# Kernel tuning notes

Hardware: AMD Instinct MI355X
Metric: run time of the kernel (lower is better)

## Reference

```python
import jax, jax.numpy as jnp
import numpy as np

C_IN, C_OUT = 256, 128

def setup_inputs() -> dict:
    key = jax.random.key(0)
    k1, k2, k3, k4, k5, k6 = jax.random.split(key, 6)
    B, H, W = 8, 64, 64
    p = jax.random.normal(k1, (B, C_IN, H, W), dtype=jnp.float32)
    b = jax.random.normal(k2, (B, C_IN, H, W), dtype=jnp.float32)
    # 1x1 conv weights (Conv2d with kernel 1 == pointwise matmul) + biases
    sq = 1.0 / np.sqrt(C_IN)
    Wq = jax.random.uniform(k3, (C_OUT, C_IN), jnp.float32, -sq, sq)
    bq = jax.random.uniform(k4, (C_OUT,), jnp.float32, -sq, sq)
    Wk = jax.random.uniform(k5, (C_OUT, C_IN), jnp.float32, -sq, sq)
    bk = jax.random.uniform(k6, (C_OUT,), jnp.float32, -sq, sq)
    return {"p": p, "b": b, "Wq": Wq, "bq": bq, "Wk": Wk, "bk": bk}

def reference(p, b, Wq, bq, Wk, bk):
    B, C, H, W = p.shape
    N = H * W
    # 1x1 convs -> flatten spatial dim to N
    q = jnp.einsum('bchw,oc->bhwo', p, Wq) + bq          # [B,H,W,Co]
    q = q.reshape(B, N, -1).astype(jnp.float32)           # [B,N,Co] (query permuted)
    k = jnp.einsum('bchw,oc->bohw', b, Wk) + bk[None, :, None, None]
    k = k.reshape(B, -1, N).astype(jnp.float32)           # [B,Co,N]
    energy = jnp.einsum('bnc,bcm->bnm', q, k)             # [B,N,N] unscaled
    attention = jax.nn.softmax(energy, axis=-1)           # softmax over keys
    value = b.reshape(B, C, N)                            # [B,C,N]
    out = jnp.einsum('bnm,bcm->bcn', attention, value)    # [B,C,N]
    return out.reshape(B, C, H, W)
```

## Files before the change

kernel.cpp:

```cpp
#include <hip/hip_runtime.h>
#include <hip/hip_bf16.h>
#include <math.h>


#define B_   8
#define CIN  256
#define COUT 128
#define NN   4096

typedef _Float16 half8  __attribute__((ext_vector_type(8)));
typedef short    short8 __attribute__((ext_vector_type(8)));
typedef float    f32x4  __attribute__((ext_vector_type(4)));

#define LOG2E 1.44269504088896340736f

__device__ __forceinline__ unsigned short f2bf(float f) {
    union { float f; unsigned u; } v; v.f = f;
    return (unsigned short)((v.u + 0x7FFFu + ((v.u >> 16) & 1u)) >> 16);
}
__device__ __forceinline__ unsigned short f2h(float f) {
    union { _Float16 h; unsigned short u; } v; v.h = (_Float16)f;
    return v.u;
}
__device__ __forceinline__ unsigned int packbf2(float lo, float hi) {
    return (unsigned int)f2bf(lo) | ((unsigned int)f2bf(hi) << 16);
}
__device__ __forceinline__ void dma16(void* lds, const void* g) {
    __builtin_amdgcn_global_load_lds(
        (const __attribute__((address_space(1))) unsigned int*)g,
        (__attribute__((address_space(3))) unsigned int*)lds,
        16, 0, 0);
}

__global__ __launch_bounds__(256) void cvt_w(const float* __restrict__ Wq,
                                             const float* __restrict__ Wk,
                                             const float* __restrict__ bq,
                                             _Float16* __restrict__ Whq,
                                             _Float16* __restrict__ Whk,
                                             float* __restrict__ bqs) {
    const int bx = blockIdx.x, t = threadIdx.x;
    const int isK = (bx >= 32);
    const float* src = isK ? Wk : Wq;
    _Float16* dst = isK ? Whk : Whq;
    const float scale = isK ? 1.0f : LOG2E;
    const int idx = (bx & 31) * 256 + t;
    float4 v = ((const float4*)src)[idx];
    unsigned long long pk = (unsigned long long)f2h(v.x * scale)
                          | ((unsigned long long)f2h(v.y * scale) << 16)
                          | ((unsigned long long)f2h(v.z * scale) << 32)
                          | ((unsigned long long)f2h(v.w * scale) << 48);
    ((unsigned long long*)dst)[idx] = pk;
    if (bx == 0 && t < COUT) bqs[t] = bq[t] * LOG2E;
}

__global__ __launch_bounds__(256) void proj3(const float* __restrict__ X,
                                             const _Float16* __restrict__ Wh,
                                             const float* __restrict__ bias,
                                             _Float16* __restrict__ outN,
                                             _Float16* __restrict__ outT,
                                             unsigned short* __restrict__ Vb)
{
    __shared__ __align__(16) unsigned short T[64 * 264];
    const int bx = blockIdx.x, b = bx >> 6, n0 = (bx & 63) << 6;
    const int t  = threadIdx.x;
    const int cr = t >> 2;
    const int nch = (t & 3) << 4;

#pragma unroll
    for (int it = 0; it < 4; ++it) {
        const int c = it * 64 + cr;
        const float* src = X + ((size_t)(b * CIN + c) * NN + n0 + nch);
        float v[16];
#pragma unroll
        for (int k = 0; k < 4; ++k) {
            float4 f = *(const float4*)(src + k * 4);
            v[k*4] = f.x; v[k*4+1] = f.y; v[k*4+2] = f.z; v[k*4+3] = f.w;
        }
#pragma unroll
        for (int j = 0; j < 16; ++j) T[(nch + j) * 264 + c] = f2h(v[j]);
        if (Vb) {
            unsigned short o[16];
#pragma unroll
            for (int j = 0; j < 16; ++j) o[j] = f2bf(v[j]);
            unsigned short* dst = Vb + (size_t)(b * CIN + c) * NN + n0 + nch;
            *(int4*)dst = *(int4*)o;
            *(int4*)(dst + 8) = *(int4*)(o + 8);
        }
    }
    __syncthreads();

    const int w = t >> 6, lane = t & 63, l15 = lane & 15, quad = lane >> 4, q8 = quad * 8;
    half8 a[8];
#pragma unroll
    for (int s = 0; s < 8; ++s)
        a[s] = *(const half8*)&T[(w * 16 + l15) * 264 + s * 32 + q8];
    f32x4 D[8];
#pragma unroll
    for (int og = 0; og < 8; ++og) D[og] = (f32x4){0.f, 0.f, 0.f, 0.f};
#pragma unroll
    for (int s = 0; s < 8; ++s) {
        const _Float16* wp = Wh + (size_t)l15 * CIN + s * 32 + q8;
#pragma unroll
        for (int og = 0; og < 8; ++og) {
            half8 wf = *(const half8*)(wp + og * 16 * CIN);
            D[og] = __builtin_amdgcn_mfma_f32_16x16x32_f16(a[s], wf, D[og], 0, 0, 0);
        }
    }
    const int nrow = n0 + w * 16 + quad * 4;
    if (outT) {
#pragma unroll
        for (int og = 0; og < 8; ++og) {
            const int o = og * 16 + l15;
            const float bo = bias[o];
            const int c = o >> 3, j = o & 7;
            const int sw = (c & 7) << 2;
#pragma unroll
            for (int r2 = 0; r2 < 4; ++r2) {
                const int n = nrow + r2;
                const int tile = n >> 5, m = n & 31;
                const size_t pos = ((size_t)(b * 128 + tile) * 512
                                    + c * 32 + ((m + sw) & 31)) * 8 + j;
                outT[pos] = (_Float16)(D[og][r2] + bo);
            }
        }
    } else {
#pragma unroll
        for (int og = 0; og < 8; ++og) {
            const int o = og * 16 + l15;
            const float bo = bias[o];
            _Float16* op = outN + ((size_t)(b * NN + nrow) * COUT + o);
#pragma unroll
            for (int r2 = 0; r2 < 4; ++r2)
                op[(size_t)r2 * COUT] = (_Float16)(D[og][r2] + bo);
        }
    }
}

__global__ __launch_bounds__(256, 2) void flash_kernel(const _Float16* __restrict__ Q,
                                                       const _Float16* __restrict__ Ktt,
                                                       const unsigned short* __restrict__ V,
                                                       float* __restrict__ out) {
    __shared__ __align__(16) _Float16       K0sh[32 * 128];
    __shared__ __align__(16) _Float16       K1sh[32 * 128];
    __shared__ __align__(16) unsigned short V0sh[256 * 32];
    __shared__ __align__(16) unsigned short V1sh[256 * 32];
    __shared__ __align__(16) unsigned short Psh[64 * 40];
    __shared__ __align__(16) float          Lsh[64];

    const int bx   = blockIdx.x;
    const int b    = bx >> 6;
    const int q0   = (bx & 63) << 6;
    const int t    = threadIdx.x;
    const int w    = t >> 6;
    const int lane = t & 63;
    const int l15  = lane & 15;
    const int quad = lane >> 4;
    const int q8   = quad * 8;

    const _Float16* Qg = Q + (size_t)b * NN * COUT;
    const _Float16* Kb = Ktt + (size_t)b * 128 * 4096;
    const unsigned short* Vg = V + (size_t)b * CIN * NN;

    half8 Qf[4];
    {
        const _Float16* qr = Qg + (size_t)(q0 + w * 16 + l15) * COUT;
#pragma unroll
        for (int s = 0; s < 4; ++s)
            Qf[s] = *(const half8*)(qr + s * 32 + q8);
    }

    f32x4 O[16];
#pragma unroll
    for (int i = 0; i < 16; ++i) O[i] = (f32x4){0.f, 0.f, 0.f, 0.f};
    float lsum[4] = {0.f, 0.f, 0.f, 0.f};

    const int vmq   = ((lane & 3) - ((lane >> 3) & 3)) & 3;
    const int vcrow = lane >> 2;
    const int vslot = (quad + (l15 >> 1)) & 3;

    auto issueK = [&](int kt, _Float16* Kd) {
        const _Float16* gk = Kb + (size_t)kt * 4096;
        dma16(Kd + (w * 2 + 0) * 512, gk + (w * 2 + 0) * 512 + lane * 8);
        dma16(Kd + (w * 2 + 1) * 512, gk + (w * 2 + 1) * 512 + lane * 8);
    };
    auto issueV = [&](int kt, unsigned short* Vd) {
        const int k0 = kt << 5;
#pragma unroll
        for (int i = 0; i < 4; ++i) {
            const int cc = (w * 4 + i) * 16 + vcrow;
            dma16(Vd + (w * 4 + i) * 512,
                  Vg + (size_t)cc * NN + k0 + vmq * 8);
        }
    };

    auto halfstep = [&](int kt, const _Float16* Kc, const unsigned short* Vc,
                        _Float16* Kn, unsigned short* Vn) {
        if (kt + 1 < 128) issueK(kt + 1, Kn);

        f32x4 S0 = {0.f, 0.f, 0.f, 0.f}, S1 = {0.f, 0.f, 0.f, 0.f};
#pragma unroll
        for (int s = 0; s < 4; ++s) {
            const int kc = 4 * s + quad;
            const int sw = (kc & 7) << 2;
            const int x0 = (l15 + sw) & 31;
            half8 kf0 = *(const half8*)(Kc + (kc * 32 + x0) * 8);
            half8 kf1 = *(const half8*)(Kc + (kc * 32 + (x0 ^ 16)) * 8);
            S0 = __builtin_amdgcn_mfma_f32_16x16x32_f16(Qf[s], kf0, S0, 0, 0, 0);
            S1 = __builtin_amdgcn_mfma_f32_16x16x32_f16(Qf[s], kf1, S1, 0, 0, 0);
        }

        f32x4 E0, E1;
#pragma unroll
        for (int r = 0; r < 4; ++r) {
            E0[r] = exp2f(S0[r]);
            E1[r] = exp2f(S1[r]);
            lsum[r] += E0[r] + E1[r];
        }
        {
            f32x4 P0, P1;
#pragma unroll
            for (int r = 0; r < 4; ++r) { P0[r] = __shfl_xor(E0[r], 1); P1[r] = __shfl_xor(E1[r], 1); }
            const int odd = l15 & 1;
            unsigned short* wp0 = Psh + w * 640
                                + (((quad << 2) + (odd << 1)) * 40) + (l15 & ~1);
            unsigned int pk0 = packbf2(odd ? P0[2] : E0[0], odd ? E0[2] : P0[0]);
            unsigned int pk1 = packbf2(odd ? P0[3] : E0[1], odd ? E0[3] : P0[1]);
            unsigned int pk2 = packbf2(odd ? P1[2] : E1[0], odd ? E1[2] : P1[0]);
            unsigned int pk3 = packbf2(odd ? P1[3] : E1[1], odd ? E1[3] : P1[1]);
            *(unsigned int*)&wp0[0]  = pk0;
            *(unsigned int*)&wp0[40] = pk1;
            *(unsigned int*)&wp0[16] = pk2;
            *(unsigned int*)&wp0[56] = pk3;
        }

        __syncthreads();

        if (kt + 1 < 128) issueV(kt + 1, Vn);

        {
            short8 pf[4];
#pragma unroll
            for (int ni = 0; ni < 4; ++ni)
                pf[ni] = *(const short8*)(Psh + (ni * 16 + l15) * 40 + q8);
            const unsigned short* vb = Vc + (w * 64 + l15) * 32 + vslot * 8;
#pragma unroll
            for (int cj = 0; cj < 4; ++cj) {
                short8 vf = *(const short8*)(vb + cj * 512);
#pragma unroll
                for (int ni = 0; ni < 4; ++ni)
                    O[ni * 4 + cj] = __builtin_amdgcn_mfma_f32_16x16x32_bf16(pf[ni], vf, O[ni * 4 + cj], 0, 0, 0);
            }
        }

        __syncthreads();
    };

    issueK(0, K0sh);
    issueV(0, V0sh);
    __syncthreads();
#pragma unroll 1
    for (int kt = 0; kt < 128; kt += 2) {
        halfstep(kt,     K0sh, V0sh, K1sh, V1sh);
        halfstep(kt + 1, K1sh, V1sh, K0sh, V0sh);
    }

#pragma unroll
    for (int r = 0; r < 4; ++r) {
        float s = lsum[r];
        s += __shfl_xor(s, 1);
        s += __shfl_xor(s, 2);
        s += __shfl_xor(s, 4);
        s += __shfl_xor(s, 8);
        if (l15 == 0) Lsh[w * 16 + (quad << 2) + r] = s;
    }
    __syncthreads();
    float* ob = out + (size_t)b * CIN * NN + q0;
#pragma unroll
    for (int ni = 0; ni < 4; ++ni) {
        const f32x4 lv = *(const f32x4*)&Lsh[ni * 16 + (quad << 2)];
        f32x4 linv;
#pragma unroll
        for (int r = 0; r < 4; ++r) linv[r] = 1.0f / lv[r];
        const int nb = ni * 16 + (quad << 2);
#pragma unroll
        for (int cj = 0; cj < 4; ++cj) {
            const int c = w * 64 + cj * 16 + l15;
            f32x4 val = O[ni * 4 + cj];
#pragma unroll
            for (int r = 0; r < 4; ++r) val[r] *= linv[r];
            *(f32x4*)(ob + (size_t)c * NN + nb) = val;
        }
    }
}

extern "C" void kernel_launch(void* const* d_in, const int* in_sizes, int n_in,
                              void* d_out, int out_size, void* d_ws, size_t ws_size,
                              hipStream_t stream) {
    const float* p  = (const float*)d_in[0];
    const float* bv = (const float*)d_in[1];
    const float* Wq = (const float*)d_in[2];
    const float* bq = (const float*)d_in[3];
    const float* Wk = (const float*)d_in[4];
    const float* bk = (const float*)d_in[5];
    float* outp = (float*)d_out;

    char* ws = (char*)d_ws;
    const size_t szQ = (size_t)B_ * NN * COUT * 2;
    const size_t szV = (size_t)B_ * NN * CIN * 2;
    const size_t szW = (size_t)COUT * CIN * 2;
    _Float16*       Qh  = (_Float16*)ws;
    _Float16*       Ktt = (_Float16*)(ws + szQ);
    unsigned short* Vb  = (unsigned short*)(ws + 2 * szQ);
    _Float16*       Whq = (_Float16*)(ws + 2 * szQ + szV);
    _Float16*       Whk = (_Float16*)(ws + 2 * szQ + szV + szW);
    float*          bqs = (float*)(ws + 2 * szQ + szV + 2 * szW);

    cvt_w<<<64, 256, 0, stream>>>(Wq, Wk, bq, Whq, Whk, bqs);
    proj3<<<512, 256, 0, stream>>>(p,  Whq, bqs, Qh, (_Float16*)nullptr, (unsigned short*)nullptr);
    proj3<<<512, 256, 0, stream>>>(bv, Whk, bk,  (_Float16*)nullptr, Ktt, Vb);
    flash_kernel<<<512, 256, 0, stream>>>(Qh, Ktt, Vb, outp);
}
```

Before: 307.5 us.

## Triple-buffer V, double-buffer P, drop a barrier, use DPP and packed bf16 cvt

The V tiles move to a three-deep ring, prefetched two steps ahead, and the P staging buffer is double-buffered. Together these let the trailing __syncthreads in each key step be removed, leaving one barrier per step. The xor-1 lane shuffle becomes a DPP move, the manual bf16 rounding is replaced by the v_cvt_pk_bf16_f32 instruction, and s_setprio raises wave priority around the MFMA blocks. In exchange, LDS use grows by about 21 KB per block, which could affect whether two blocks fit per CU, and correctness now depends on the buffer rotation being hazard-free.

```diff
diff --git a/kernel.cpp b/kernel.cpp
--- a/kernel.cpp
+++ b/kernel.cpp
@@ -22,8 +22,15 @@
     union { _Float16 h; unsigned short u; } v; v.h = (_Float16)f;
     return v.u;
 }
-__device__ __forceinline__ unsigned int packbf2(float lo, float hi) {
-    return (unsigned int)f2bf(lo) | ((unsigned int)f2bf(hi) << 16);
+__device__ __forceinline__ unsigned int cvt_pk_bf16(float lo, float hi) {
+    unsigned int r;
+    asm("v_cvt_pk_bf16_f32 %0, %1, %2" : "=v"(r) : "v"(lo), "v"(hi));
+    return r;
+}
+__device__ __forceinline__ float dpp_xor1(float x) {
+    union { float f; int i; } u; u.f = x;
+    u.i = __builtin_amdgcn_mov_dpp(u.i, 0xB1, 0xF, 0xF, true);
+    return u.f;
 }
 __device__ __forceinline__ void dma16(void* lds, const void* g) {
     __builtin_amdgcn_global_load_lds(
@@ -144,7 +151,9 @@
     __shared__ __align__(16) _Float16       K1sh[32 * 128];
     __shared__ __align__(16) unsigned short V0sh[256 * 32];
     __shared__ __align__(16) unsigned short V1sh[256 * 32];
-    __shared__ __align__(16) unsigned short Psh[64 * 40];
+    __shared__ __align__(16) unsigned short V2sh[256 * 32];
+    __shared__ __align__(16) unsigned short P0sh[64 * 40];
+    __shared__ __align__(16) unsigned short P1sh[64 * 40];
     __shared__ __align__(16) float          Lsh[64];
 
     const int bx   = blockIdx.x;
@@ -193,11 +202,13 @@
         }
     };
 
-    auto halfstep = [&](int kt, const _Float16* Kc, const unsigned short* Vc,
-                        _Float16* Kn, unsigned short* Vn) {
+    auto halfstep = [&](int kt, const _Float16* Kc, _Float16* Kn,
+                        const unsigned short* Va, unsigned short* Vn2,
+                        unsigned short* Pc) {
         if (kt + 1 < 128) issueK(kt + 1, Kn);
 
         f32x4 S0 = {0.f, 0.f, 0.f, 0.f}, S1 = {0.f, 0.f, 0.f, 0.f};
+        __builtin_amdgcn_s_setprio(1);
 #pragma unroll
         for (int s = 0; s < 4; ++s) {
             const int kc = 4 * s + quad;
@@ -208,6 +219,7 @@
             S0 = __builtin_amdgcn_mfma_f32_16x16x32_f16(Qf[s], kf0, S0, 0, 0, 0);
             S1 = __builtin_amdgcn_mfma_f32_16x16x32_f16(Qf[s], kf1, S1, 0, 0, 0);
         }
+        __builtin_amdgcn_s_setprio(0);
 
         f32x4 E0, E1;
 #pragma unroll
@@ -219,14 +231,14 @@
         {
             f32x4 P0, P1;
 #pragma unroll
-            for (int r = 0; r < 4; ++r) { P0[r] = __shfl_xor(E0[r], 1); P1[r] = __shfl_xor(E1[r], 1); }
+            for (int r = 0; r < 4; ++r) { P0[r] = dpp_xor1(E0[r]); P1[r] = dpp_xor1(E1[r]); }
             const int odd = l15 & 1;
-            unsigned short* wp0 = Psh + w * 640
+            unsigned short* wp0 = Pc + w * 640
                                 + (((quad << 2) + (odd << 1)) * 40) + (l15 & ~1);
-            unsigned int pk0 = packbf2(odd ? P0[2] : E0[0], odd ? E0[2] : P0[0]);
-            unsigned int pk1 = packbf2(odd ? P0[3] : E0[1], odd ? E0[3] : P0[1]);
-            unsigned int pk2 = packbf2(odd ? P1[2] : E1[0], odd ? E1[2] : P1[0]);
-            unsigned int pk3 = packbf2(odd ? P1[3] : E1[1], odd ? E1[3] : P1[1]);
+            unsigned int pk0 = cvt_pk_bf16(odd ? P0[2] : E0[0], odd ? E0[2] : P0[0]);
+            unsigned int pk1 = cvt_pk_bf16(odd ? P0[3] : E0[1], odd ? E0[3] : P0[1]);
+            unsigned int pk2 = cvt_pk_bf16(odd ? P1[2] : E1[0], odd ? E1[2] : P1[0]);
+            unsigned int pk3 = cvt_pk_bf16(odd ? P1[3] : E1[1], odd ? E1[3] : P1[1]);
             *(unsigned int*)&wp0[0]  = pk0;
             *(unsigned int*)&wp0[40] = pk1;
             *(unsigned int*)&wp0[16] = pk2;
@@ -235,14 +247,15 @@
 
         __syncthreads();
 
-        if (kt + 1 < 128) issueV(kt + 1, Vn);
+        if (kt + 2 < 128) issueV(kt + 2, Vn2);
 
         {
             short8 pf[4];
 #pragma unroll
             for (int ni = 0; ni < 4; ++ni)
-                pf[ni] = *(const short8*)(Psh + (ni * 16 + l15) * 40 + q8);
-            const unsigned short* vb = Vc + (w * 64 + l15) * 32 + vslot * 8;
+                pf[ni] = *(const short8*)(Pc + (ni * 16 + l15) * 40 + q8);
+            const unsigned short* vb = Va + (w * 64 + l15) * 32 + vslot * 8;
+            __builtin_amdgcn_s_setprio(1);
 #pragma unroll
             for (int cj = 0; cj < 4; ++cj) {
                 short8 vf = *(const short8*)(vb + cj * 512);
@@ -250,18 +263,24 @@
                 for (int ni = 0; ni < 4; ++ni)
                     O[ni * 4 + cj] = __builtin_amdgcn_mfma_f32_16x16x32_bf16(pf[ni], vf, O[ni * 4 + cj], 0, 0, 0);
             }
-        }
-
-        __syncthreads();
+            __builtin_amdgcn_s_setprio(0);
+        }
     };
 
     issueK(0, K0sh);
     issueV(0, V0sh);
+    issueV(1, V1sh);
     __syncthreads();
+
+    _Float16*       Kc = K0sh; _Float16*       Kn = K1sh;
+    unsigned short* Va = V0sh; unsigned short* Vm = V1sh; unsigned short* Vn2 = V2sh;
+    unsigned short* Pc = P0sh; unsigned short* Pn = P1sh;
 #pragma unroll 1
-    for (int kt = 0; kt < 128; kt += 2) {
-        halfstep(kt,     K0sh, V0sh, K1sh, V1sh);
-        halfstep(kt + 1, K1sh, V1sh, K0sh, V0sh);
+    for (int kt = 0; kt < 128; ++kt) {
+        halfstep(kt, Kc, Kn, Va, Vn2, Pc);
+        _Float16* tk = Kc; Kc = Kn; Kn = tk;
+        unsigned short* tv = Va; Va = Vm; Vm = Vn2; Vn2 = tv;
+        unsigned short* tp = Pc; Pc = Pn; Pn = tp;
     }
 
 #pragma unroll
```

Result: faster. 284.4 us (-7.5%).
